# Kernel tuning notes

Measured on AMD Instinct MI355X. Metric: run time of the kernel, lower is better.

The kernel has to match this reference:

```python
import jax, jax.numpy as jnp
import numpy as np

B, S, D = 8, 4096, 1024
N_LEVELS = 8
L = 8
EPS = 1e-3        # FSQ eps (bound shrink)
LN_EPS = 1e-5     # torch LayerNorm default eps


def setup_inputs() -> dict:
    key = jax.random.key(0)
    k1, k2 = jax.random.split(key)
    regrs = jax.random.normal(k1, (B, S, D), dtype=jnp.float32)
    ln_w = jnp.ones((D,), dtype=jnp.float32)
    ln_b = jnp.zeros((D,), dtype=jnp.float32)
    # nn.Linear(d_model, n_levels, bias=False): weight shape [n_levels, d_model]
    W = jax.random.normal(k2, (N_LEVELS, D), dtype=jnp.float32) * (1.0 / np.sqrt(D))
    return {"regrs": regrs, "ln_w": ln_w, "ln_b": ln_b, "W": W}


def reference(regrs, ln_w, ln_b, W):
    # LayerNorm over last dim (biased variance, matching torch)
    mean = jnp.mean(regrs, axis=-1, keepdims=True)
    var = jnp.mean(jnp.square(regrs - mean), axis=-1, keepdims=True)
    x = (regrs - mean) * jax.lax.rsqrt(var + LN_EPS) * ln_w + ln_b
    # skinny projection to n_levels channels
    z = jnp.einsum('bsd,nd->bsn', x, W)  # [B,S,N_LEVELS]
    half_l = L * (1.0 - EPS) / 2.0
    bounded = half_l * jnp.tanh(z)
    # round with straight-through estimator
    code = bounded + jax.lax.stop_gradient(jnp.round(bounded) - bounded)
    return code
```

## Files before the change

kernel.cpp:

```cpp
#include <hip/hip_runtime.h>
#include <math.h>

#define NLEV 8
#define D_DIM 1024

struct TB  { float  t[8]; };
struct TBD { double t[8]; };

template<int CTRL>
__device__ __forceinline__ float ror_add(float v) {
    int r = __builtin_amdgcn_update_dpp(0, __float_as_int(v), CTRL, 0xF, 0xF, true);
    return v + __int_as_float(r);
}
__device__ __forceinline__ float red16(float v) {
    v = ror_add<0x121>(v);
    v = ror_add<0x122>(v);
    v = ror_add<0x124>(v);
    v = ror_add<0x128>(v);
    return v;
}
__device__ __forceinline__ float wave_allreduce(float v) {
    v = red16(v);
    v += __shfl_xor(v, 16, 64);
    v += __shfl_xor(v, 32, 64);
    return v;
}

__global__ __launch_bounds__(256, 4) void fsq_main(
        const float* __restrict__ xg,
        const float* __restrict__ gg,
        const float* __restrict__ bg,
        const float* __restrict__ Wg,
        float* __restrict__ outg,
        unsigned int* __restrict__ wl,
        int wl_cap, int nrows, TB tb)
{
    __shared__ float Vs[NLEV][D_DIM];
    __shared__ float redc1[4][NLEV];
    __shared__ float redc0[4][NLEV];

    const int tid  = (int)threadIdx.x;
    const int lane = tid & 63;
    const int wv   = tid >> 6;

    {
        const int col = tid * 4;
        const float4 g4 = *(const float4*)(gg + col);
        const float4 b4 = *(const float4*)(bg + col);
        #pragma unroll
        for (int n = 0; n < NLEV; ++n) {
            const float4 w4 = *(const float4*)(Wg + n * D_DIM + col);
            float4 v4;
            v4.x = g4.x * w4.x; v4.y = g4.y * w4.y;
            v4.z = g4.z * w4.z; v4.w = g4.w * w4.w;
            *(float4*)&Vs[n][col] = v4;
            float c1 = wave_allreduce((v4.x + v4.y) + (v4.z + v4.w));
            float c0 = wave_allreduce((b4.x * w4.x + b4.y * w4.y)
                                    + (b4.z * w4.z + b4.w * w4.w));
            if (lane == 0) { redc1[wv][n] = c1; redc0[wv][n] = c0; }
        }
    }
    __syncthreads();
    const int nsel = lane & 7;
    const float C1sel = redc1[0][nsel] + redc1[1][nsel] + redc1[2][nsel] + redc1[3][nsel];
    const float C0sel = redc0[0][nsel] + redc0[1][nsel] + redc0[2][nsel] + redc0[3][nsel];

    const long wave_row0 = (long)blockIdx.x * 32 + (long)wv * 8;
    const float4* xb = (const float4*)xg;

    for (int p = 0; p < 4; ++p) {
        const long r0 = wave_row0 + 2 * p;
        if (r0 >= nrows) break;
        const long base0 = r0 * (D_DIM / 4) + lane;
        float4 xv0[4], xv1[4];
        #pragma unroll
        for (int j = 0; j < 4; ++j) xv0[j] = xb[base0 + j * 64];
        #pragma unroll
        for (int j = 0; j < 4; ++j) xv1[j] = xb[base0 + 256 + j * 64];

        float s0 = 0.f, s1 = 0.f, sq0 = 0.f, sq1 = 0.f;
        float acc0[NLEV], acc1[NLEV];
        #pragma unroll
        for (int n = 0; n < NLEV; ++n) { acc0[n] = 0.f; acc1[n] = 0.f; }

        #pragma unroll
        for (int j = 0; j < 4; ++j) {
            const int vcol = j * 256 + lane * 4;
            const float4 a = xv0[j];
            const float4 b = xv1[j];
            s0 += (a.x + a.y) + (a.z + a.w);
            s1 += (b.x + b.y) + (b.z + b.w);
            sq0 = fmaf(a.x, a.x, sq0); sq0 = fmaf(a.y, a.y, sq0);
            sq0 = fmaf(a.z, a.z, sq0); sq0 = fmaf(a.w, a.w, sq0);
            sq1 = fmaf(b.x, b.x, sq1); sq1 = fmaf(b.y, b.y, sq1);
            sq1 = fmaf(b.z, b.z, sq1); sq1 = fmaf(b.w, b.w, sq1);
            #pragma unroll
            for (int n = 0; n < NLEV; ++n) {
                const float4 v4 = *(const float4*)&Vs[n][vcol];
                acc0[n] = fmaf(a.x, v4.x, acc0[n]);
                acc0[n] = fmaf(a.y, v4.y, acc0[n]);
                acc0[n] = fmaf(a.z, v4.z, acc0[n]);
                acc0[n] = fmaf(a.w, v4.w, acc0[n]);
                acc1[n] = fmaf(b.x, v4.x, acc1[n]);
                acc1[n] = fmaf(b.y, v4.y, acc1[n]);
                acc1[n] = fmaf(b.z, v4.z, acc1[n]);
                acc1[n] = fmaf(b.w, v4.w, acc1[n]);
            }
        }

        s0 = red16(s0); s1 = red16(s1); sq0 = red16(sq0); sq1 = red16(sq1);
        #pragma unroll
        for (int n = 0; n < NLEV; ++n) { acc0[n] = red16(acc0[n]); acc1[n] = red16(acc1[n]); }

        float u0, u1, u2, u3, w0, w1;
        u0 = (lane & 4) ? acc0[4] : acc0[0];
        u1 = (lane & 4) ? acc0[5] : acc0[1];
        u2 = (lane & 4) ? acc0[6] : acc0[2];
        u3 = (lane & 4) ? acc0[7] : acc0[3];
        w0 = (lane & 2) ? u2 : u0;
        w1 = (lane & 2) ? u3 : u1;
        float S0 = (lane & 1) ? w1 : w0;
        u0 = (lane & 4) ? acc1[4] : acc1[0];
        u1 = (lane & 4) ? acc1[5] : acc1[1];
        u2 = (lane & 4) ? acc1[6] : acc1[2];
        u3 = (lane & 4) ? acc1[7] : acc1[3];
        w0 = (lane & 2) ? u2 : u0;
        w1 = (lane & 2) ? u3 : u1;
        float S1 = (lane & 1) ? w1 : w0;

        S0  += __shfl_xor(S0, 16, 64);  S0  += __shfl_xor(S0, 32, 64);
        S1  += __shfl_xor(S1, 16, 64);  S1  += __shfl_xor(S1, 32, 64);
        s0  += __shfl_xor(s0, 16, 64);  s0  += __shfl_xor(s0, 32, 64);
        s1  += __shfl_xor(s1, 16, 64);  s1  += __shfl_xor(s1, 32, 64);
        sq0 += __shfl_xor(sq0, 16, 64); sq0 += __shfl_xor(sq0, 32, 64);
        sq1 += __shfl_xor(sq1, 16, 64); sq1 += __shfl_xor(sq1, 32, 64);

        bool flag = false;
        if (lane < 16) {
            const long row = (lane < 8) ? r0 : (r0 + 1);
            if (row < nrows) {
                const float S  = (lane < 8) ? S0  : S1;
                const float ss = (lane < 8) ? s0  : s1;
                const float qq = (lane < 8) ? sq0 : sq1;
                const float mean = ss * (1.0f / 1024.0f);
                const float var  = qq * (1.0f / 1024.0f) - mean * mean;
                const float rstd = 1.0f / sqrtf(var + 1e-5f);
                const float z = rstd * (S - mean * C1sel) + C0sel;
                int cnt = 0;
                float mind = 1e30f;
                #pragma unroll
                for (int k = 0; k < 8; ++k) {
                    cnt += (z > tb.t[k]) ? 1 : 0;
                    mind = fminf(mind, fabsf(z - tb.t[k]));
                }
                outg[row * NLEV + nsel] = (float)(cnt - 4);
                flag = (mind < 1.0e-3f);
            }
        }
        const unsigned long long bal = __ballot(flag);
        if (lane == 0 && bal != 0ULL) {
            if (bal & 0xFFull) {
                const unsigned i = atomicAdd(wl, 1u);
                if (i < (unsigned)wl_cap) wl[16 + i] = (unsigned)r0;
            }
            if (bal & 0xFF00ull) {
                const unsigned i = atomicAdd(wl, 1u);
                if (i < (unsigned)wl_cap) wl[16 + i] = (unsigned)(r0 + 1);
            }
        }
    }
}

__global__ __launch_bounds__(256, 1) void fsq_fix(
        const float* __restrict__ xg,
        const float* __restrict__ gg,
        const float* __restrict__ bg,
        const float* __restrict__ Wg,
        float* __restrict__ outg,
        const unsigned int* __restrict__ wl,
        int wl_cap, TBD tbd)
{
    const int tid  = (int)threadIdx.x;
    const int lane = tid & 63;
    const int wv   = tid >> 6;
    const unsigned wave   = blockIdx.x * 4 + wv;
    const unsigned nwaves = gridDim.x * 4;

    unsigned cnt = wl[0];
    if (cnt > (unsigned)wl_cap) cnt = (unsigned)wl_cap;
    if (wave >= cnt) return;

    for (unsigned it = wave; it < cnt; it += nwaves) {
        const long row = (long)wl[16 + it];
        const float4* xb4 = (const float4*)(xg + row * D_DIM);

        float4 xr[4];
        #pragma unroll
        for (int j = 0; j < 4; ++j) xr[j] = xb4[j * 64 + lane];

        double s = 0.0, sq = 0.0;
        #pragma unroll
        for (int j = 0; j < 4; ++j) {
            const double x0 = (double)xr[j].x, x1 = (double)xr[j].y;
            const double x2 = (double)xr[j].z, x3 = (double)xr[j].w;
            s += ((x0 + x1) + (x2 + x3));
            sq = fma(x0, x0, sq); sq = fma(x1, x1, sq);
            sq = fma(x2, x2, sq); sq = fma(x3, x3, sq);
        }
        #pragma unroll
        for (int off = 32; off >= 1; off >>= 1) {
            s  += __shfl_xor(s, off, 64);
            sq += __shfl_xor(sq, off, 64);
        }
        const double mean = s * (1.0 / 1024.0);
        const double var  = sq * (1.0 / 1024.0) - mean * mean;
        const double rstd = 1.0 / sqrt(var + 1e-5);

        double acc[NLEV];
        #pragma unroll
        for (int n = 0; n < NLEV; ++n) acc[n] = 0.0;
        #pragma unroll
        for (int j = 0; j < 4; ++j) {
            const int col = j * 256 + lane * 4;
            const float4 g4 = *(const float4*)(gg + col);
            const float4 b4 = *(const float4*)(bg + col);
            const double y0 = fma(((double)xr[j].x - mean) * rstd, (double)g4.x, (double)b4.x);
            const double y1 = fma(((double)xr[j].y - mean) * rstd, (double)g4.y, (double)b4.y);
            const double y2 = fma(((double)xr[j].z - mean) * rstd, (double)g4.z, (double)b4.z);
            const double y3 = fma(((double)xr[j].w - mean) * rstd, (double)g4.w, (double)b4.w);
            #pragma unroll
            for (int n = 0; n < NLEV; ++n) {
                const float4 w4 = *(const float4*)(Wg + n * D_DIM + col);
                acc[n] = fma(y0, (double)w4.x, acc[n]);
                acc[n] = fma(y1, (double)w4.y, acc[n]);
                acc[n] = fma(y2, (double)w4.z, acc[n]);
                acc[n] = fma(y3, (double)w4.w, acc[n]);
            }
        }
        #pragma unroll
        for (int off = 32; off >= 1; off >>= 1) {
            #pragma unroll
            for (int n = 0; n < NLEV; ++n) acc[n] += __shfl_xor(acc[n], off, 64);
        }

        if (lane < NLEV) {
            double a0 = (lane & 4) ? acc[4] : acc[0];
            double a1 = (lane & 4) ? acc[5] : acc[1];
            double a2 = (lane & 4) ? acc[6] : acc[2];
            double a3 = (lane & 4) ? acc[7] : acc[3];
            double b0 = (lane & 2) ? a2 : a0;
            double b1 = (lane & 2) ? a3 : a1;
            const double z = (lane & 1) ? b1 : b0;
            int c = 0;
            #pragma unroll
            for (int k = 0; k < 8; ++k) c += (z > tbd.t[k]) ? 1 : 0;
            outg[row * NLEV + lane] = (float)(c - 4);
        }
    }
}

extern "C" void kernel_launch(void* const* d_in, const int* in_sizes, int n_in,
                              void* d_out, int out_size, void* d_ws, size_t ws_size,
                              hipStream_t stream) {
    (void)n_in; (void)out_size;
    const float* regrs = (const float*)d_in[0];
    const float* ln_w  = (const float*)d_in[1];
    const float* ln_b  = (const float*)d_in[2];
    const float* W     = (const float*)d_in[3];
    float* out = (float*)d_out;

    const int nrows = in_sizes[0] / D_DIM;
    const int nblocks = (nrows + 31) / 32;

    unsigned int* wl = (unsigned int*)d_ws;
    long cap_l = ((long)(ws_size / 4)) - 16;
    if (cap_l < 0) cap_l = 0;
    if (cap_l > nrows) cap_l = nrows;
    const int wl_cap = (int)cap_l;

    TB tb; TBD tbd;
    for (int k = 0; k < 8; ++k) {
        const double y = ((double)k - 3.5) / 3.996;
        tbd.t[k] = atanh(y);
        tb.t[k]  = (float)tbd.t[k];
    }

    hipMemsetAsync(d_ws, 0, 64, stream);
    fsq_main<<<nblocks, 256, 0, stream>>>(regrs, ln_w, ln_b, W, out, wl, wl_cap, nrows, tb);
    fsq_fix<<<64, 256, 0, stream>>>(regrs, ln_w, ln_b, W, out, wl, wl_cap, tbd);
}
```

Measured before the change: 227.3 us.

## Fuse double-precision fixup into main kernel and prefetch next row pair

Removes the workspace memset, the atomic worklist and the separate fsq_fix launch. Rows whose projection lands near a rounding threshold are now recomputed in double precision inline by the same wave. The row loop also software-prefetches the next pair of rows into registers while the current pair is processed, and the per-level wave reductions are batched after the loads. This drops two extra launches and the serialization between them, at the cost of more register pressure and divergent inline fixups. It also removes the nrows bounds checks, so it assumes the row count is a multiple of 32.

```diff
diff --git a/kernel.cpp b/kernel.cpp
--- a/kernel.cpp
+++ b/kernel.cpp
@@ -26,14 +26,13 @@
     return v;
 }
 
-__global__ __launch_bounds__(256, 4) void fsq_main(
+__global__ __launch_bounds__(256, 4) void fsq_fused(
         const float* __restrict__ xg,
         const float* __restrict__ gg,
         const float* __restrict__ bg,
         const float* __restrict__ Wg,
         float* __restrict__ outg,
-        unsigned int* __restrict__ wl,
-        int wl_cap, int nrows, TB tb)
+        int nrows, TB tb, TBD tbd)
 {
     __shared__ float Vs[NLEV][D_DIM];
     __shared__ float redc1[4][NLEV];
@@ -47,6 +46,7 @@
         const int col = tid * 4;
         const float4 g4 = *(const float4*)(gg + col);
         const float4 b4 = *(const float4*)(bg + col);
+        float pc1[NLEV], pc0[NLEV];
         #pragma unroll
         for (int n = 0; n < NLEV; ++n) {
             const float4 w4 = *(const float4*)(Wg + n * D_DIM + col);
@@ -54,10 +54,17 @@
             v4.x = g4.x * w4.x; v4.y = g4.y * w4.y;
             v4.z = g4.z * w4.z; v4.w = g4.w * w4.w;
             *(float4*)&Vs[n][col] = v4;
-            float c1 = wave_allreduce((v4.x + v4.y) + (v4.z + v4.w));
-            float c0 = wave_allreduce((b4.x * w4.x + b4.y * w4.y)
-                                    + (b4.z * w4.z + b4.w * w4.w));
-            if (lane == 0) { redc1[wv][n] = c1; redc0[wv][n] = c0; }
+            pc1[n] = (v4.x + v4.y) + (v4.z + v4.w);
+            pc0[n] = (b4.x * w4.x + b4.y * w4.y) + (b4.z * w4.z + b4.w * w4.w);
+        }
+        #pragma unroll
+        for (int n = 0; n < NLEV; ++n) {
+            pc1[n] = wave_allreduce(pc1[n]);
+            pc0[n] = wave_allreduce(pc0[n]);
+        }
+        if (lane == 0) {
+            #pragma unroll
+            for (int n = 0; n < NLEV; ++n) { redc1[wv][n] = pc1[n]; redc0[wv][n] = pc0[n]; }
         }
     }
     __syncthreads();
@@ -67,16 +74,25 @@
 
     const long wave_row0 = (long)blockIdx.x * 32 + (long)wv * 8;
     const float4* xb = (const float4*)xg;
+    const long base0 = wave_row0 * (D_DIM / 4) + lane;
+
+    float4 xv0[4], xv1[4];
+    #pragma unroll
+    for (int j = 0; j < 4; ++j) xv0[j] = xb[base0 + j * 64];
+    #pragma unroll
+    for (int j = 0; j < 4; ++j) xv1[j] = xb[base0 + 256 + j * 64];
 
     for (int p = 0; p < 4; ++p) {
         const long r0 = wave_row0 + 2 * p;
-        if (r0 >= nrows) break;
-        const long base0 = r0 * (D_DIM / 4) + lane;
-        float4 xv0[4], xv1[4];
-        #pragma unroll
-        for (int j = 0; j < 4; ++j) xv0[j] = xb[base0 + j * 64];
-        #pragma unroll
-        for (int j = 0; j < 4; ++j) xv1[j] = xb[base0 + 256 + j * 64];
+
+        float4 xn0[4], xn1[4];
+        if (p < 3) {
+            const long nb = base0 + (long)(p + 1) * 512;
+            #pragma unroll
+            for (int j = 0; j < 4; ++j) xn0[j] = xb[nb + j * 64];
+            #pragma unroll
+            for (int j = 0; j < 4; ++j) xn1[j] = xb[nb + 256 + j * 64];
+        }
 
         float s0 = 0.f, s1 = 0.f, sq0 = 0.f, sq1 = 0.f;
         float acc0[NLEV], acc1[NLEV];
@@ -137,124 +153,100 @@
 
         bool flag = false;
         if (lane < 16) {
+            const float S  = (lane < 8) ? S0  : S1;
+            const float ss = (lane < 8) ? s0  : s1;
+            const float qq = (lane < 8) ? sq0 : sq1;
             const long row = (lane < 8) ? r0 : (r0 + 1);
-            if (row < nrows) {
-                const float S  = (lane < 8) ? S0  : S1;
-                const float ss = (lane < 8) ? s0  : s1;
-                const float qq = (lane < 8) ? sq0 : sq1;
-                const float mean = ss * (1.0f / 1024.0f);
-                const float var  = qq * (1.0f / 1024.0f) - mean * mean;
-                const float rstd = 1.0f / sqrtf(var + 1e-5f);
-                const float z = rstd * (S - mean * C1sel) + C0sel;
-                int cnt = 0;
-                float mind = 1e30f;
-                #pragma unroll
-                for (int k = 0; k < 8; ++k) {
-                    cnt += (z > tb.t[k]) ? 1 : 0;
-                    mind = fminf(mind, fabsf(z - tb.t[k]));
-                }
-                outg[row * NLEV + nsel] = (float)(cnt - 4);
-                flag = (mind < 1.0e-3f);
+            const float mean = ss * (1.0f / 1024.0f);
+            const float var  = qq * (1.0f / 1024.0f) - mean * mean;
+            const float rstd = 1.0f / sqrtf(var + 1e-5f);
+            const float z = rstd * (S - mean * C1sel) + C0sel;
+            int cnt = 0;
+            float mind = 1e30f;
+            #pragma unroll
+            for (int k = 0; k < 8; ++k) {
+                cnt += (z > tb.t[k]) ? 1 : 0;
+                mind = fminf(mind, fabsf(z - tb.t[k]));
             }
+            outg[row * NLEV + nsel] = (float)(cnt - 4);
+            flag = (mind < 1.0e-3f);
         }
         const unsigned long long bal = __ballot(flag);
-        if (lane == 0 && bal != 0ULL) {
-            if (bal & 0xFFull) {
-                const unsigned i = atomicAdd(wl, 1u);
-                if (i < (unsigned)wl_cap) wl[16 + i] = (unsigned)r0;
+
+        if (bal != 0ULL) {
+            #pragma unroll 1
+            for (int half = 0; half < 2; ++half) {
+                if (!(bal & (half ? 0xFF00ull : 0x00FFull))) continue;
+                const long row = r0 + half;
+                const float4* xb4 = (const float4*)(xg + row * D_DIM);
+
+                float4 xr[4];
+                #pragma unroll
+                for (int j = 0; j < 4; ++j) xr[j] = xb4[j * 64 + lane];
+
+                double s = 0.0, sq = 0.0;
+                #pragma unroll
+                for (int j = 0; j < 4; ++j) {
+                    const double x0 = (double)xr[j].x, x1 = (double)xr[j].y;
+                    const double x2 = (double)xr[j].z, x3 = (double)xr[j].w;
+                    s += ((x0 + x1) + (x2 + x3));
+                    sq = fma(x0, x0, sq); sq = fma(x1, x1, sq);
+                    sq = fma(x2, x2, sq); sq = fma(x3, x3, sq);
+                }
+                #pragma unroll
+                for (int off = 32; off >= 1; off >>= 1) {
+                    s  += __shfl_xor(s, off, 64);
+                    sq += __shfl_xor(sq, off, 64);
+                }
+                const double mean = s * (1.0 / 1024.0);
+                const double var  = sq * (1.0 / 1024.0) - mean * mean;
+                const double rstd = 1.0 / sqrt(var + 1e-5);
+
+                double acc[NLEV];
+                #pragma unroll
+                for (int n = 0; n < NLEV; ++n) acc[n] = 0.0;
+                #pragma unroll
+                for (int j = 0; j < 4; ++j) {
+                    const int col = j * 256 + lane * 4;
+                    const float4 g4 = *(const float4*)(gg + col);
+                    const float4 b4 = *(const float4*)(bg + col);
+                    const double y0 = fma(((double)xr[j].x - mean) * rstd, (double)g4.x, (double)b4.x);
+                    const double y1 = fma(((double)xr[j].y - mean) * rstd, (double)g4.y, (double)b4.y);
+                    const double y2 = fma(((double)xr[j].z - mean) * rstd, (double)g4.z, (double)b4.z);
+                    const double y3 = fma(((double)xr[j].w - mean) * rstd, (double)g4.w, (double)b4.w);
+                    #pragma unroll
+                    for (int n = 0; n < NLEV; ++n) {
+                        const float4 w4 = *(const float4*)(Wg + n * D_DIM + col);
+                        acc[n] = fma(y0, (double)w4.x, acc[n]);
+                        acc[n] = fma(y1, (double)w4.y, acc[n]);
+                        acc[n] = fma(y2, (double)w4.z, acc[n]);
+                        acc[n] = fma(y3, (double)w4.w, acc[n]);
+                    }
+                }
+                #pragma unroll
+                for (int off = 32; off >= 1; off >>= 1) {
+                    #pragma unroll
+                    for (int n = 0; n < NLEV; ++n) acc[n] += __shfl_xor(acc[n], off, 64);
+                }
+                if (lane < NLEV) {
+                    double a0 = (lane & 4) ? acc[4] : acc[0];
+                    double a1 = (lane & 4) ? acc[5] : acc[1];
+                    double a2 = (lane & 4) ? acc[6] : acc[2];
+                    double a3 = (lane & 4) ? acc[7] : acc[3];
+                    double b0 = (lane & 2) ? a2 : a0;
+                    double b1 = (lane & 2) ? a3 : a1;
+                    const double z = (lane & 1) ? b1 : b0;
+                    int c = 0;
+                    #pragma unroll
+                    for (int k = 0; k < 8; ++k) c += (z > tbd.t[k]) ? 1 : 0;
+                    outg[row * NLEV + lane] = (float)(c - 4);
+                }
             }
-            if (bal & 0xFF00ull) {
-                const unsigned i = atomicAdd(wl, 1u);
-                if (i < (unsigned)wl_cap) wl[16 + i] = (unsigned)(r0 + 1);
-            }
-        }
-    }
-}
-
-__global__ __launch_bounds__(256, 1) void fsq_fix(
-        const float* __restrict__ xg,
-        const float* __restrict__ gg,
-        const float* __restrict__ bg,
-        const float* __restrict__ Wg,
-        float* __restrict__ outg,
-        const unsigned int* __restrict__ wl,
-        int wl_cap, TBD tbd)
-{
-    const int tid  = (int)threadIdx.x;
-    const int lane = tid & 63;
-    const int wv   = tid >> 6;
-    const unsigned wave   = blockIdx.x * 4 + wv;
-    const unsigned nwaves = gridDim.x * 4;
-
-    unsigned cnt = wl[0];
-    if (cnt > (unsigned)wl_cap) cnt = (unsigned)wl_cap;
-    if (wave >= cnt) return;
-
-    for (unsigned it = wave; it < cnt; it += nwaves) {
-        const long row = (long)wl[16 + it];
-        const float4* xb4 = (const float4*)(xg + row * D_DIM);
-
-        float4 xr[4];
-        #pragma unroll
-        for (int j = 0; j < 4; ++j) xr[j] = xb4[j * 64 + lane];
-
-        double s = 0.0, sq = 0.0;
-        #pragma unroll
-        for (int j = 0; j < 4; ++j) {
-            const double x0 = (double)xr[j].x, x1 = (double)xr[j].y;
-            const double x2 = (double)xr[j].z, x3 = (double)xr[j].w;
-            s += ((x0 + x1) + (x2 + x3));
-            sq = fma(x0, x0, sq); sq = fma(x1, x1, sq);
-            sq = fma(x2, x2, sq); sq = fma(x3, x3, sq);
-        }
-        #pragma unroll
-        for (int off = 32; off >= 1; off >>= 1) {
-            s  += __shfl_xor(s, off, 64);
-            sq += __shfl_xor(sq, off, 64);
-        }
-        const double mean = s * (1.0 / 1024.0);
-        const double var  = sq * (1.0 / 1024.0) - mean * mean;
-        const double rstd = 1.0 / sqrt(var + 1e-5);
-
-        double acc[NLEV];
-        #pragma unroll
-        for (int n = 0; n < NLEV; ++n) acc[n] = 0.0;
-        #pragma unroll
-        for (int j = 0; j < 4; ++j) {
-            const int col = j * 256 + lane * 4;
-            const float4 g4 = *(const float4*)(gg + col);
-            const float4 b4 = *(const float4*)(bg + col);
-            const double y0 = fma(((double)xr[j].x - mean) * rstd, (double)g4.x, (double)b4.x);
-            const double y1 = fma(((double)xr[j].y - mean) * rstd, (double)g4.y, (double)b4.y);
-            const double y2 = fma(((double)xr[j].z - mean) * rstd, (double)g4.z, (double)b4.z);
-            const double y3 = fma(((double)xr[j].w - mean) * rstd, (double)g4.w, (double)b4.w);
-            #pragma unroll
-            for (int n = 0; n < NLEV; ++n) {
-                const float4 w4 = *(const float4*)(Wg + n * D_DIM + col);
-                acc[n] = fma(y0, (double)w4.x, acc[n]);
-                acc[n] = fma(y1, (double)w4.y, acc[n]);
-                acc[n] = fma(y2, (double)w4.z, acc[n]);
-                acc[n] = fma(y3, (double)w4.w, acc[n]);
-            }
-        }
-        #pragma unroll
-        for (int off = 32; off >= 1; off >>= 1) {
-            #pragma unroll
-            for (int n = 0; n < NLEV; ++n) acc[n] += __shfl_xor(acc[n], off, 64);
-        }
-
-        if (lane < NLEV) {
-            double a0 = (lane & 4) ? acc[4] : acc[0];
-            double a1 = (lane & 4) ? acc[5] : acc[1];
-            double a2 = (lane & 4) ? acc[6] : acc[2];
-            double a3 = (lane & 4) ? acc[7] : acc[3];
-            double b0 = (lane & 2) ? a2 : a0;
-            double b1 = (lane & 2) ? a3 : a1;
-            const double z = (lane & 1) ? b1 : b0;
-            int c = 0;
-            #pragma unroll
-            for (int k = 0; k < 8; ++k) c += (z > tbd.t[k]) ? 1 : 0;
-            outg[row * NLEV + lane] = (float)(c - 4);
+        }
+
+        if (p < 3) {
+            #pragma unroll
+            for (int j = 0; j < 4; ++j) { xv0[j] = xn0[j]; xv1[j] = xn1[j]; }
         }
     }
 }
@@ -262,7 +254,7 @@
 extern "C" void kernel_launch(void* const* d_in, const int* in_sizes, int n_in,
                               void* d_out, int out_size, void* d_ws, size_t ws_size,
                               hipStream_t stream) {
-    (void)n_in; (void)out_size;
+    (void)n_in; (void)out_size; (void)d_ws; (void)ws_size;
     const float* regrs = (const float*)d_in[0];
     const float* ln_w  = (const float*)d_in[1];
     const float* ln_b  = (const float*)d_in[2];
@@ -271,12 +263,6 @@
 
     const int nrows = in_sizes[0] / D_DIM;
     const int nblocks = (nrows + 31) / 32;
-
-    unsigned int* wl = (unsigned int*)d_ws;
-    long cap_l = ((long)(ws_size / 4)) - 16;
-    if (cap_l < 0) cap_l = 0;
-    if (cap_l > nrows) cap_l = nrows;
-    const int wl_cap = (int)cap_l;
 
     TB tb; TBD tbd;
     for (int k = 0; k < 8; ++k) {
@@ -285,7 +271,5 @@
         tb.t[k]  = (float)tbd.t[k];
     }
 
-    hipMemsetAsync(d_ws, 0, 64, stream);
-    fsq_main<<<nblocks, 256, 0, stream>>>(regrs, ln_w, ln_b, W, out, wl, wl_cap, nrows, tb);
-    fsq_fix<<<64, 256, 0, stream>>>(regrs, ln_w, ln_b, W, out, wl, wl_cap, tbd);
-}
+    fsq_fused<<<nblocks, 256, 0, stream>>>(regrs, ln_w, ln_b, W, out, nrows, tb, tbd);
+}
```

After: 488.3 us. +114.9%, slower.

## Process one row per wave iteration and batch setup reductions to cut register pressure

Applied to the files above, without the earlier changes.

The main kernel now handles a single row per loop iteration instead of two interleaved rows. This halves accumulator and x-register usage and removes the min-occupancy launch bound, letting the compiler pick register allocation. Setup constant reductions are batched after all loads. The fix kernel reloads x from global instead of holding it in registers, and its grid is doubled. The trade-off is less memory-level parallelism per wave (one row of loads in flight instead of two) in exchange for potentially higher occupancy.

```diff
diff --git a/kernel.cpp b/kernel.cpp
--- a/kernel.cpp
+++ b/kernel.cpp
@@ -26,7 +26,7 @@
     return v;
 }
 
-__global__ __launch_bounds__(256, 4) void fsq_main(
+__global__ __launch_bounds__(256) void fsq_main(
         const float* __restrict__ xg,
         const float* __restrict__ gg,
         const float* __restrict__ bg,
@@ -47,6 +47,7 @@
         const int col = tid * 4;
         const float4 g4 = *(const float4*)(gg + col);
         const float4 b4 = *(const float4*)(bg + col);
+        float pc1[NLEV], pc0[NLEV];
         #pragma unroll
         for (int n = 0; n < NLEV; ++n) {
             const float4 w4 = *(const float4*)(Wg + n * D_DIM + col);
@@ -54,10 +55,17 @@
             v4.x = g4.x * w4.x; v4.y = g4.y * w4.y;
             v4.z = g4.z * w4.z; v4.w = g4.w * w4.w;
             *(float4*)&Vs[n][col] = v4;
-            float c1 = wave_allreduce((v4.x + v4.y) + (v4.z + v4.w));
-            float c0 = wave_allreduce((b4.x * w4.x + b4.y * w4.y)
-                                    + (b4.z * w4.z + b4.w * w4.w));
-            if (lane == 0) { redc1[wv][n] = c1; redc0[wv][n] = c0; }
+            pc1[n] = (v4.x + v4.y) + (v4.z + v4.w);
+            pc0[n] = (b4.x * w4.x + b4.y * w4.y) + (b4.z * w4.z + b4.w * w4.w);
+        }
+        #pragma unroll
+        for (int n = 0; n < NLEV; ++n) {
+            pc1[n] = wave_allreduce(pc1[n]);
+            pc0[n] = wave_allreduce(pc0[n]);
+        }
+        if (lane == 0) {
+            #pragma unroll
+            for (int n = 0; n < NLEV; ++n) { redc1[wv][n] = pc1[n]; redc0[wv][n] = pc0[n]; }
         }
     }
     __syncthreads();
@@ -68,110 +76,79 @@
     const long wave_row0 = (long)blockIdx.x * 32 + (long)wv * 8;
     const float4* xb = (const float4*)xg;
 
-    for (int p = 0; p < 4; ++p) {
-        const long r0 = wave_row0 + 2 * p;
-        if (r0 >= nrows) break;
-        const long base0 = r0 * (D_DIM / 4) + lane;
-        float4 xv0[4], xv1[4];
-        #pragma unroll
-        for (int j = 0; j < 4; ++j) xv0[j] = xb[base0 + j * 64];
-        #pragma unroll
-        for (int j = 0; j < 4; ++j) xv1[j] = xb[base0 + 256 + j * 64];
-
-        float s0 = 0.f, s1 = 0.f, sq0 = 0.f, sq1 = 0.f;
-        float acc0[NLEV], acc1[NLEV];
-        #pragma unroll
-        for (int n = 0; n < NLEV; ++n) { acc0[n] = 0.f; acc1[n] = 0.f; }
+    for (int p = 0; p < 8; ++p) {
+        const long row = wave_row0 + p;
+        if (row >= nrows) break;
+
+        const float4* xr = xb + row * (D_DIM / 4);
+        float4 xv0 = xr[lane];
+        float4 xv1 = xr[64 + lane];
+        float4 xv2 = xr[128 + lane];
+        float4 xv3 = xr[192 + lane];
+
+        float s = 0.f, sq = 0.f;
+        float acc[NLEV];
+        #pragma unroll
+        for (int n = 0; n < NLEV; ++n) acc[n] = 0.f;
 
         #pragma unroll
         for (int j = 0; j < 4; ++j) {
+            const float4 a = (j == 0) ? xv0 : (j == 1) ? xv1 : (j == 2) ? xv2 : xv3;
             const int vcol = j * 256 + lane * 4;
-            const float4 a = xv0[j];
-            const float4 b = xv1[j];
-            s0 += (a.x + a.y) + (a.z + a.w);
-            s1 += (b.x + b.y) + (b.z + b.w);
-            sq0 = fmaf(a.x, a.x, sq0); sq0 = fmaf(a.y, a.y, sq0);
-            sq0 = fmaf(a.z, a.z, sq0); sq0 = fmaf(a.w, a.w, sq0);
-            sq1 = fmaf(b.x, b.x, sq1); sq1 = fmaf(b.y, b.y, sq1);
-            sq1 = fmaf(b.z, b.z, sq1); sq1 = fmaf(b.w, b.w, sq1);
+            s += (a.x + a.y) + (a.z + a.w);
+            sq = fmaf(a.x, a.x, sq); sq = fmaf(a.y, a.y, sq);
+            sq = fmaf(a.z, a.z, sq); sq = fmaf(a.w, a.w, sq);
             #pragma unroll
             for (int n = 0; n < NLEV; ++n) {
                 const float4 v4 = *(const float4*)&Vs[n][vcol];
-                acc0[n] = fmaf(a.x, v4.x, acc0[n]);
-                acc0[n] = fmaf(a.y, v4.y, acc0[n]);
-                acc0[n] = fmaf(a.z, v4.z, acc0[n]);
-                acc0[n] = fmaf(a.w, v4.w, acc0[n]);
-                acc1[n] = fmaf(b.x, v4.x, acc1[n]);
-                acc1[n] = fmaf(b.y, v4.y, acc1[n]);
-                acc1[n] = fmaf(b.z, v4.z, acc1[n]);
-                acc1[n] = fmaf(b.w, v4.w, acc1[n]);
+                acc[n] = fmaf(a.x, v4.x, acc[n]);
+                acc[n] = fmaf(a.y, v4.y, acc[n]);
+                acc[n] = fmaf(a.z, v4.z, acc[n]);
+                acc[n] = fmaf(a.w, v4.w, acc[n]);
             }
         }
 
-        s0 = red16(s0); s1 = red16(s1); sq0 = red16(sq0); sq1 = red16(sq1);
-        #pragma unroll
-        for (int n = 0; n < NLEV; ++n) { acc0[n] = red16(acc0[n]); acc1[n] = red16(acc1[n]); }
-
-        float u0, u1, u2, u3, w0, w1;
-        u0 = (lane & 4) ? acc0[4] : acc0[0];
-        u1 = (lane & 4) ? acc0[5] : acc0[1];
-        u2 = (lane & 4) ? acc0[6] : acc0[2];
-        u3 = (lane & 4) ? acc0[7] : acc0[3];
-        w0 = (lane & 2) ? u2 : u0;
-        w1 = (lane & 2) ? u3 : u1;
-        float S0 = (lane & 1) ? w1 : w0;
-        u0 = (lane & 4) ? acc1[4] : acc1[0];
-        u1 = (lane & 4) ? acc1[5] : acc1[1];
-        u2 = (lane & 4) ? acc1[6] : acc1[2];
-        u3 = (lane & 4) ? acc1[7] : acc1[3];
-        w0 = (lane & 2) ? u2 : u0;
-        w1 = (lane & 2) ? u3 : u1;
-        float S1 = (lane & 1) ? w1 : w0;
-
-        S0  += __shfl_xor(S0, 16, 64);  S0  += __shfl_xor(S0, 32, 64);
-        S1  += __shfl_xor(S1, 16, 64);  S1  += __shfl_xor(S1, 32, 64);
-        s0  += __shfl_xor(s0, 16, 64);  s0  += __shfl_xor(s0, 32, 64);
-        s1  += __shfl_xor(s1, 16, 64);  s1  += __shfl_xor(s1, 32, 64);
-        sq0 += __shfl_xor(sq0, 16, 64); sq0 += __shfl_xor(sq0, 32, 64);
-        sq1 += __shfl_xor(sq1, 16, 64); sq1 += __shfl_xor(sq1, 32, 64);
+        s = red16(s); sq = red16(sq);
+        #pragma unroll
+        for (int n = 0; n < NLEV; ++n) acc[n] = red16(acc[n]);
+
+        float u0 = (lane & 4) ? acc[4] : acc[0];
+        float u1 = (lane & 4) ? acc[5] : acc[1];
+        float u2 = (lane & 4) ? acc[6] : acc[2];
+        float u3 = (lane & 4) ? acc[7] : acc[3];
+        float w0 = (lane & 2) ? u2 : u0;
+        float w1 = (lane & 2) ? u3 : u1;
+        float Ssel = (lane & 1) ? w1 : w0;
+
+        Ssel += __shfl_xor(Ssel, 16, 64); Ssel += __shfl_xor(Ssel, 32, 64);
+        s    += __shfl_xor(s, 16, 64);    s    += __shfl_xor(s, 32, 64);
+        sq   += __shfl_xor(sq, 16, 64);   sq   += __shfl_xor(sq, 32, 64);
 
         bool flag = false;
-        if (lane < 16) {
-            const long row = (lane < 8) ? r0 : (r0 + 1);
-            if (row < nrows) {
-                const float S  = (lane < 8) ? S0  : S1;
-                const float ss = (lane < 8) ? s0  : s1;
-                const float qq = (lane < 8) ? sq0 : sq1;
-                const float mean = ss * (1.0f / 1024.0f);
-                const float var  = qq * (1.0f / 1024.0f) - mean * mean;
-                const float rstd = 1.0f / sqrtf(var + 1e-5f);
-                const float z = rstd * (S - mean * C1sel) + C0sel;
-                int cnt = 0;
-                float mind = 1e30f;
-                #pragma unroll
-                for (int k = 0; k < 8; ++k) {
-                    cnt += (z > tb.t[k]) ? 1 : 0;
-                    mind = fminf(mind, fabsf(z - tb.t[k]));
-                }
-                outg[row * NLEV + nsel] = (float)(cnt - 4);
-                flag = (mind < 1.0e-3f);
+        if (lane < NLEV) {
+            const float mean = s * (1.0f / 1024.0f);
+            const float var  = sq * (1.0f / 1024.0f) - mean * mean;
+            const float rstd = 1.0f / sqrtf(var + 1e-5f);
+            const float z = rstd * (Ssel - mean * C1sel) + C0sel;
+            int cnt = 0;
+            float mind = 1e30f;
+            #pragma unroll
+            for (int k = 0; k < 8; ++k) {
+                cnt += (z > tb.t[k]) ? 1 : 0;
+                mind = fminf(mind, fabsf(z - tb.t[k]));
             }
+            outg[row * NLEV + lane] = (float)(cnt - 4);
+            flag = (mind < 1.0e-3f);
         }
         const unsigned long long bal = __ballot(flag);
         if (lane == 0 && bal != 0ULL) {
-            if (bal & 0xFFull) {
-                const unsigned i = atomicAdd(wl, 1u);
-                if (i < (unsigned)wl_cap) wl[16 + i] = (unsigned)r0;
-            }
-            if (bal & 0xFF00ull) {
-                const unsigned i = atomicAdd(wl, 1u);
-                if (i < (unsigned)wl_cap) wl[16 + i] = (unsigned)(r0 + 1);
-            }
-        }
-    }
-}
-
-__global__ __launch_bounds__(256, 1) void fsq_fix(
+            const unsigned i = atomicAdd(wl, 1u);
+            if (i < (unsigned)wl_cap) wl[16 + i] = (unsigned)row;
+        }
+    }
+}
+
+__global__ __launch_bounds__(256) void fsq_fix(
         const float* __restrict__ xg,
         const float* __restrict__ gg,
         const float* __restrict__ bg,
@@ -194,15 +171,12 @@
         const long row = (long)wl[16 + it];
         const float4* xb4 = (const float4*)(xg + row * D_DIM);
 
-        float4 xr[4];
-        #pragma unroll
-        for (int j = 0; j < 4; ++j) xr[j] = xb4[j * 64 + lane];
-
         double s = 0.0, sq = 0.0;
         #pragma unroll
         for (int j = 0; j < 4; ++j) {
-            const double x0 = (double)xr[j].x, x1 = (double)xr[j].y;
-            const double x2 = (double)xr[j].z, x3 = (double)xr[j].w;
+            const float4 x4 = xb4[j * 64 + lane];
+            const double x0 = (double)x4.x, x1 = (double)x4.y;
+            const double x2 = (double)x4.z, x3 = (double)x4.w;
             s += ((x0 + x1) + (x2 + x3));
             sq = fma(x0, x0, sq); sq = fma(x1, x1, sq);
             sq = fma(x2, x2, sq); sq = fma(x3, x3, sq);
@@ -222,12 +196,13 @@
         #pragma unroll
         for (int j = 0; j < 4; ++j) {
             const int col = j * 256 + lane * 4;
+            const float4 x4 = xb4[j * 64 + lane];
             const float4 g4 = *(const float4*)(gg + col);
             const float4 b4 = *(const float4*)(bg + col);
-            const double y0 = fma(((double)xr[j].x - mean) * rstd, (double)g4.x, (double)b4.x);
-            const double y1 = fma(((double)xr[j].y - mean) * rstd, (double)g4.y, (double)b4.y);
-            const double y2 = fma(((double)xr[j].z - mean) * rstd, (double)g4.z, (double)b4.z);
-            const double y3 = fma(((double)xr[j].w - mean) * rstd, (double)g4.w, (double)b4.w);
+            const double y0 = fma(((double)x4.x - mean) * rstd, (double)g4.x, (double)b4.x);
+            const double y1 = fma(((double)x4.y - mean) * rstd, (double)g4.y, (double)b4.y);
+            const double y2 = fma(((double)x4.z - mean) * rstd, (double)g4.z, (double)b4.z);
+            const double y3 = fma(((double)x4.w - mean) * rstd, (double)g4.w, (double)b4.w);
             #pragma unroll
             for (int n = 0; n < NLEV; ++n) {
                 const float4 w4 = *(const float4*)(Wg + n * D_DIM + col);
@@ -287,5 +262,5 @@
 
     hipMemsetAsync(d_ws, 0, 64, stream);
     fsq_main<<<nblocks, 256, 0, stream>>>(regrs, ln_w, ln_b, W, out, wl, wl_cap, nrows, tb);
-    fsq_fix<<<64, 256, 0, stream>>>(regrs, ln_w, ln_b, W, out, wl, wl_cap, tbd);
-}
+    fsq_fix<<<128, 256, 0, stream>>>(regrs, ln_w, ln_b, W, out, wl, wl_cap, tbd);
+}
```

Measured after the change: 218.7 us. -3.8%, faster.
